# Optimization experiments

Measured on AMD Instinct MI355X. Metric: run time of the kernel, lower is better.

Reference implementation:

```python
import jax, jax.numpy as jnp
import numpy as np

BETA_VQ = 0.25
NUM_CODES = 1024
CODE_DIM = 256

def setup_inputs() -> dict:
    key = jax.random.key(0)
    k1, k2 = jax.random.split(key)
    z_e = jax.random.normal(k1, (64, 32, 32, CODE_DIM), dtype=jnp.float32)
    codebook = jax.random.uniform(k2, (NUM_CODES, CODE_DIM), dtype=jnp.float32,
                                  minval=-1.0 / NUM_CODES, maxval=1.0 / NUM_CODES)
    return {"z_e": z_e, "codebook": codebook}


def reference(z_e, codebook):
    B, H, W, D = z_e.shape
    z_flat = z_e.reshape(-1, D)  # [N, D], N = B*H*W
    # squared-euclidean distances via expansion: ||z||^2 + ||c||^2 - 2 z.c
    dist = (jnp.sum(z_flat ** 2, axis=1, keepdims=True)
            + jnp.sum(codebook ** 2, axis=1)
            - 2.0 * z_flat @ codebook.T)  # [N, num_codes]
    indices = jnp.argmin(dist, axis=1)  # [N]
    z_q = codebook[indices].reshape(z_e.shape)  # [B,H,W,D]
    codebook_loss = jnp.mean((jax.lax.stop_gradient(z_e) - z_q) ** 2)
    commit_loss = BETA_VQ * jnp.mean((z_e - jax.lax.stop_gradient(z_q)) ** 2)
    vq_loss = codebook_loss + commit_loss
    z_q_st = z_e + jax.lax.stop_gradient(z_q - z_e)  # straight-through
    indices = indices.reshape(B, H, W)
    return (z_q_st, vq_loss, indices)
```

## Files before the change

kernel.cpp:

```cpp
#include <hip/hip_runtime.h>
#include <hip/hip_bf16.h>


constexpr int D     = 256;
constexpr int NC    = 1024;
constexpr int NROWS = 65536;
constexpr int RPB   = 32;
constexpr int NBLK  = NROWS / RPB;
constexpr int ZS    = 264;
constexpr int QCAP  = 1024;
#define MARGIN_Q 3.8e-3f

typedef float accv4  __attribute__((ext_vector_type(4)));
typedef short short8 __attribute__((ext_vector_type(8)));

__device__ __forceinline__ short f2bf(float x) {
    __hip_bfloat16 h = __float2bfloat16(x);
    return *reinterpret_cast<short*>(&h);
}
__device__ __forceinline__ unsigned packtrunc(float x, float y) {
    return (__float_as_uint(x) >> 16) | (__float_as_uint(y) & 0xffff0000u);
}

__device__ __forceinline__ float np_pairwise_sq128(const float* __restrict__ x) {
    float r[8];
    #pragma unroll
    for (int j = 0; j < 8; ++j) r[j] = __fmul_rn(x[j], x[j]);
    #pragma unroll
    for (int i = 8; i < 128; i += 8)
        #pragma unroll
        for (int j = 0; j < 8; ++j)
            r[j] = __fadd_rn(r[j], __fmul_rn(x[i + j], x[i + j]));
    float s01 = __fadd_rn(r[0], r[1]);
    float s23 = __fadd_rn(r[2], r[3]);
    float s45 = __fadd_rn(r[4], r[5]);
    float s67 = __fadd_rn(r[6], r[7]);
    return __fadd_rn(__fadd_rn(s01, s23), __fadd_rn(s45, s67));
}

__global__ void c2_kernel(const float* __restrict__ cb, float* __restrict__ c2) {
    int t = blockIdx.x * blockDim.x + threadIdx.x;
    if (t < NC) {
        const float* x = cb + (size_t)t * D;
        c2[t] = __fadd_rn(np_pairwise_sq128(x), np_pairwise_sq128(x + 128));
    }
}

__global__ void swz_kernel(const float* __restrict__ cb, short* __restrict__ swz) {
    int t = blockIdx.x * blockDim.x + threadIdx.x;
    int lane = t & 63, ts = t >> 6;
    int ks = ts & 7, tile = ts >> 3;
    int code = tile * 16 + (lane & 15);
    int kb   = ks * 32 + (lane >> 4) * 8;
    const float* src = cb + (size_t)code * D + kb;
    union { short s[8]; short8 v; } u;
    #pragma unroll
    for (int j = 0; j < 8; ++j) u.s[j] = f2bf(src[j]);
    *((short8*)swz + t) = u.v;
}

__global__ __launch_bounds__(256, 2) void vq_kernel(
    const float* __restrict__ z,
    const float* __restrict__ cb,
    const short* __restrict__ cb_swz,
    const float* __restrict__ c2g,
    float*       __restrict__ out_zq,
    float*       __restrict__ out_idx,
    double*      __restrict__ partials)
{
    __shared__ __align__(16) float z_lds[RPB][ZS];
    __shared__ float a_row[RPB];
    __shared__ __align__(16) float scratchA[RPB][4];
    __shared__ float c2_lds[NC];
    __shared__ int   rm_shared[RPB];
    __shared__ __align__(16) int queue[QCAP];
    __shared__ int   qn;

    const int tid     = threadIdx.x;
    const int lane    = tid & 63;
    const int w       = tid >> 6;
    const int rowBase = blockIdx.x * RPB;

    #pragma unroll
    for (int j = 0; j < 8; ++j) {
        int l = tid + 256 * j;
        int row = l >> 6, q = l & 63;
        float4 v = *(const float4*)(z + (size_t)(rowBase + row) * D + q * 4);
        *(float4*)&z_lds[row][q * 4] = v;
    }
    #pragma unroll
    for (int j = 0; j < 4; ++j) c2_lds[tid + 256 * j] = c2g[tid + 256 * j];
    if (tid < RPB) rm_shared[tid] = 0x7f800000;
    if (tid == 0)  qn = 0;
    __syncthreads();

    if (tid < RPB * 4) {
        int row = tid >> 2, q = tid & 3;
        int h = (q >> 1) * 128, p = (q & 1) * 4;
        const float* x = &z_lds[row][0];
        float r0 = __fmul_rn(x[h+p+0], x[h+p+0]);
        float r1 = __fmul_rn(x[h+p+1], x[h+p+1]);
        float r2 = __fmul_rn(x[h+p+2], x[h+p+2]);
        float r3 = __fmul_rn(x[h+p+3], x[h+p+3]);
        #pragma unroll
        for (int i = 8; i < 128; i += 8) {
            r0 = __fadd_rn(r0, __fmul_rn(x[h+i+p+0], x[h+i+p+0]));
            r1 = __fadd_rn(r1, __fmul_rn(x[h+i+p+1], x[h+i+p+1]));
            r2 = __fadd_rn(r2, __fmul_rn(x[h+i+p+2], x[h+i+p+2]));
            r3 = __fadd_rn(r3, __fmul_rn(x[h+i+p+3], x[h+i+p+3]));
        }
        scratchA[row][q] = __fadd_rn(__fadd_rn(r0, r1), __fadd_rn(r2, r3));
    }
    __syncthreads();
    if (tid < RPB) {
        float half0 = __fadd_rn(scratchA[tid][0], scratchA[tid][1]);
        float half1 = __fadd_rn(scratchA[tid][2], scratchA[tid][3]);
        a_row[tid]  = __fadd_rn(half0, half1);
    }
    __syncthreads();

    short8 afrag[2][8];
    #pragma unroll
    for (int rt = 0; rt < 2; ++rt)
        #pragma unroll
        for (int ks = 0; ks < 8; ++ks) {
            const float* src = z + (size_t)(rowBase + rt * 16 + (lane & 15)) * D
                                 + ks * 32 + (lane >> 4) * 8;
            float4 v0 = *(const float4*)(src);
            float4 v1 = *(const float4*)(src + 4);
            union { unsigned u[4]; short8 v; } pk;
            pk.u[0] = packtrunc(v0.x, v0.y);
            pk.u[1] = packtrunc(v0.z, v0.w);
            pk.u[2] = packtrunc(v1.x, v1.y);
            pk.u[3] = packtrunc(v1.z, v1.w);
            afrag[rt][ks] = pk.v;
        }
    float a_reg[2][4];
    #pragma unroll
    for (int rt = 0; rt < 2; ++rt)
        #pragma unroll
        for (int i = 0; i < 4; ++i)
            a_reg[rt][i] = a_row[rt * 16 + (lane >> 4) * 4 + i];

    float runmin[2][4];
    #pragma unroll
    for (int rt = 0; rt < 2; ++rt)
        #pragma unroll
        for (int i = 0; i < 4; ++i) runmin[rt][i] = 3.4e38f;

    const short8* bbase = (const short8*)cb_swz + lane;
    short8 bcur[8];
    #pragma unroll
    for (int ks = 0; ks < 8; ++ks) bcur[ks] = bbase[(size_t)w * 512 + ks * 64];

    unsigned kpk[2][2][2];
    #pragma unroll
    for (int t = 0; t < 2; ++t) {
        const int tile = w + 4 * t;
        short8 bnxt[8];
        #pragma unroll
        for (int ks = 0; ks < 8; ++ks)
            bnxt[ks] = bbase[(size_t)(tile + 4) * 512 + ks * 64];
        accv4 acc[2];
        #pragma unroll
        for (int rt = 0; rt < 2; ++rt) acc[rt] = (accv4){0.f, 0.f, 0.f, 0.f};
        #pragma unroll
        for (int ks = 0; ks < 8; ++ks) {
            #pragma unroll
            for (int rt = 0; rt < 2; ++rt)
                acc[rt] = __builtin_amdgcn_mfma_f32_16x16x32_bf16(
                    afrag[rt][ks], bcur[ks], acc[rt], 0, 0, 0);
        }
        const float c2v = c2_lds[tile * 16 + (lane & 15)];
        #pragma unroll
        for (int rt = 0; rt < 2; ++rt) {
            float m0 = fmaf(2.0f, acc[rt][0], -c2v);
            float m1 = fmaf(2.0f, acc[rt][1], -c2v);
            float m2 = fmaf(2.0f, acc[rt][2], -c2v);
            float m3 = fmaf(2.0f, acc[rt][3], -c2v);
            kpk[t][rt][0] = packtrunc(m0, m1);
            kpk[t][rt][1] = packtrunc(m2, m3);
            runmin[rt][0] = fminf(runmin[rt][0], a_reg[rt][0] - m0);
            runmin[rt][1] = fminf(runmin[rt][1], a_reg[rt][1] - m1);
            runmin[rt][2] = fminf(runmin[rt][2], a_reg[rt][2] - m2);
            runmin[rt][3] = fminf(runmin[rt][3], a_reg[rt][3] - m3);
        }
        #pragma unroll
        for (int ks = 0; ks < 8; ++ks) bcur[ks] = bnxt[ks];
    }

    #pragma unroll
    for (int rt = 0; rt < 2; ++rt)
        #pragma unroll
        for (int i = 0; i < 4; ++i) {
            float m = runmin[rt][i];
            m = fminf(m, __shfl_xor(m, 1));
            m = fminf(m, __shfl_xor(m, 2));
            m = fminf(m, __shfl_xor(m, 4));
            m = fminf(m, __shfl_xor(m, 8));
            if ((lane & 15) == 0) {
                int row = rt * 16 + (lane >> 4) * 4 + i;
                atomicMin(&rm_shared[row], __float_as_int(m));
            }
        }
    __syncthreads();

    float mthr[2][4];
    #pragma unroll
    for (int rt = 0; rt < 2; ++rt)
        #pragma unroll
        for (int i = 0; i < 4; ++i) {
            int row = rt * 16 + (lane >> 4) * 4 + i;
            mthr[rt][i] = a_reg[rt][i]
                        - (__int_as_float(rm_shared[row]) + MARGIN_Q);
        }

    #pragma unroll
    for (int t = 0; t < 2; ++t) {
        const int code = (w + 4 * t) * 16 + (lane & 15);
        #pragma unroll
        for (int rt = 0; rt < 2; ++rt)
            #pragma unroll
            for (int pr = 0; pr < 2; ++pr) {
                unsigned pk = kpk[t][rt][pr];
                float mlo = __uint_as_float(pk << 16);
                float mhi = __uint_as_float(pk & 0xffff0000u);
                if (mlo >= mthr[rt][2 * pr]) {
                    int row  = rt * 16 + (lane >> 4) * 4 + 2 * pr;
                    int slot = atomicAdd(&qn, 1);
                    if (slot < QCAP) queue[slot] = (row << 10) | code;
                }
                if (mhi >= mthr[rt][2 * pr + 1]) {
                    int row  = rt * 16 + (lane >> 4) * 4 + 2 * pr + 1;
                    int slot = atomicAdd(&qn, 1);
                    if (slot < QCAP) queue[slot] = (row << 10) | code;
                }
            }
    }

    for (int t = 2; t < 16; ++t) {
        const int tile = w + 4 * t;
        short8 bnxt[8];
        if (t < 15) {
            #pragma unroll
            for (int ks = 0; ks < 8; ++ks)
                bnxt[ks] = bbase[(size_t)(tile + 4) * 512 + ks * 64];
        }
        accv4 acc[2];
        #pragma unroll
        for (int rt = 0; rt < 2; ++rt) acc[rt] = (accv4){0.f, 0.f, 0.f, 0.f};
        #pragma unroll
        for (int ks = 0; ks < 8; ++ks) {
            #pragma unroll
            for (int rt = 0; rt < 2; ++rt)
                acc[rt] = __builtin_amdgcn_mfma_f32_16x16x32_bf16(
                    afrag[rt][ks], bcur[ks], acc[rt], 0, 0, 0);
        }
        const float c2v  = c2_lds[tile * 16 + (lane & 15)];
        const int   code = tile * 16 + (lane & 15);
        #pragma unroll
        for (int rt = 0; rt < 2; ++rt) {
            #pragma unroll
            for (int i = 0; i < 4; ++i) {
                float m = fmaf(2.0f, acc[rt][i], -c2v);
                runmin[rt][i] = fminf(runmin[rt][i], a_reg[rt][i] - m);
                if (m >= mthr[rt][i]) {
                    int row  = rt * 16 + (lane >> 4) * 4 + i;
                    int slot = atomicAdd(&qn, 1);
                    if (slot < QCAP) queue[slot] = (row << 10) | code;
                }
            }
        }
        if (t == 5 || t == 9 || t == 13) {
            #pragma unroll
            for (int rt = 0; rt < 2; ++rt)
                #pragma unroll
                for (int i = 0; i < 4; ++i) {
                    float m = runmin[rt][i];
                    m = fminf(m, __shfl_xor(m, 1));
                    m = fminf(m, __shfl_xor(m, 2));
                    m = fminf(m, __shfl_xor(m, 4));
                    m = fminf(m, __shfl_xor(m, 8));
                    if ((lane & 15) == 0) {
                        int row = rt * 16 + (lane >> 4) * 4 + i;
                        atomicMin(&rm_shared[row], __float_as_int(m));
                    }
                }
            #pragma unroll
            for (int rt = 0; rt < 2; ++rt)
                #pragma unroll
                for (int i = 0; i < 4; ++i) {
                    int row = rt * 16 + (lane >> 4) * 4 + i;
                    mthr[rt][i] = a_reg[rt][i]
                                - (__int_as_float(rm_shared[row]) + MARGIN_Q);
                }
        }
        if (t < 15) {
            #pragma unroll
            for (int ks = 0; ks < 8; ++ks) bcur[ks] = bnxt[ks];
        }
    }

    unsigned long long* best64 = (unsigned long long*)&scratchA[0][0];
    if (tid < RPB) best64[tid] = ~0ull;
    __syncthreads();
    int total = qn;
    if (total <= QCAP) {
        for (int t = tid; t < total; t += 256) {
            int e = queue[t];
            int row = e >> 10, code = e & 1023;
            const float4* cp = (const float4*)(cb + (size_t)code * D);
            const float*  zr = &z_lds[row][0];
            float acc = 0.0f;
            #pragma unroll 8
            for (int d4 = 0; d4 < 64; ++d4) {
                float4 cv = cp[d4];
                acc = fmaf(zr[d4 * 4 + 0], cv.x, acc);
                acc = fmaf(zr[d4 * 4 + 1], cv.y, acc);
                acc = fmaf(zr[d4 * 4 + 2], cv.z, acc);
                acc = fmaf(zr[d4 * 4 + 3], cv.w, acc);
            }
            float key = __fsub_rn(__fadd_rn(a_row[row], c2_lds[code]), 2.0f * acc);
            unsigned long long pk =
                ((unsigned long long)__float_as_uint(key) << 32) | (unsigned)code;
            atomicMin(&best64[row], pk);
        }
    } else {
        for (int r = 0; r < RPB; ++r) {
            for (int c = tid; c < NC; c += 256) {
                const float4* cp = (const float4*)(cb + (size_t)c * D);
                const float*  zr = &z_lds[r][0];
                float acc = 0.0f;
                #pragma unroll 8
                for (int d4 = 0; d4 < 64; ++d4) {
                    float4 cv = cp[d4];
                    acc = fmaf(zr[d4 * 4 + 0], cv.x, acc);
                    acc = fmaf(zr[d4 * 4 + 1], cv.y, acc);
                    acc = fmaf(zr[d4 * 4 + 2], cv.z, acc);
                    acc = fmaf(zr[d4 * 4 + 3], cv.w, acc);
                }
                float key = __fsub_rn(__fadd_rn(a_row[r], c2_lds[c]), 2.0f * acc);
                unsigned long long pk =
                    ((unsigned long long)__float_as_uint(key) << 32) | (unsigned)c;
                atomicMin(&best64[r], pk);
            }
        }
    }
    __syncthreads();

    int* winner = rm_shared;
    if (tid < RPB) {
        unsigned long long b = best64[tid];
        int wdx = (b == ~0ull) ? 0 : (int)(b & 0xffffffffu);
        winner[tid] = wdx;
        out_idx[rowBase + tid] = (float)wdx;
    }
    __syncthreads();

    double lacc = 0.0;
    #pragma unroll
    for (int j = 0; j < 8; ++j) {
        int idx = tid + 256 * j;
        int row = idx >> 6;
        int q4  = idx & 63;
        int wd  = winner[row];
        float4 cv = *(const float4*)(cb + (size_t)wd * D + q4 * 4);
        float4 zv = *(const float4*)&z_lds[row][q4 * 4];
        float4 o;
        o.x = __fadd_rn(zv.x, __fsub_rn(cv.x, zv.x));
        o.y = __fadd_rn(zv.y, __fsub_rn(cv.y, zv.y));
        o.z = __fadd_rn(zv.z, __fsub_rn(cv.z, zv.z));
        o.w = __fadd_rn(zv.w, __fsub_rn(cv.w, zv.w));
        *(float4*)(out_zq + (size_t)(rowBase + row) * D + q4 * 4) = o;
        double d0 = (double)zv.x - (double)cv.x;
        double d1 = (double)zv.y - (double)cv.y;
        double d2 = (double)zv.z - (double)cv.z;
        double d3 = (double)zv.w - (double)cv.w;
        lacc += d0 * d0 + d1 * d1 + d2 * d2 + d3 * d3;
    }
    __syncthreads();
    double* dred = (double*)&queue[0];
    dred[tid] = lacc;
    __syncthreads();
    for (int s = 128; s > 0; s >>= 1) {
        if (tid < s) dred[tid] += dred[tid + s];
        __syncthreads();
    }
    if (tid == 0) partials[blockIdx.x] = dred[0];
}

__global__ void loss_kernel(const double* __restrict__ partials,
                            float* __restrict__ out_loss)
{
    __shared__ double sm[256];
    int tid = threadIdx.x;
    double s = 0.0;
    for (int i = tid; i < NBLK; i += 256) s += partials[i];
    sm[tid] = s;
    __syncthreads();
    for (int k = 128; k > 0; k >>= 1) {
        if (tid < k) sm[tid] += sm[tid + k];
        __syncthreads();
    }
    if (tid == 0)
        out_loss[0] = (float)(1.25 * sm[0] / (double)((size_t)NROWS * D));
}

extern "C" void kernel_launch(void* const* d_in, const int* in_sizes, int n_in,
                              void* d_out, int out_size, void* d_ws, size_t ws_size,
                              hipStream_t stream)
{
    const float* z  = (const float*)d_in[0];
    const float* cb = (const float*)d_in[1];

    float* out      = (float*)d_out;
    float* out_zq   = out;
    float* out_loss = out + (size_t)NROWS * D;
    float* out_idx  = out_loss + 1;

    char*   ws       = (char*)d_ws;
    short*  cb_swz   = (short*)ws;
    float*  c2       = (float*)(ws + 524288);
    double* partials = (double*)(ws + 528384);

    swz_kernel<<<128, 256, 0, stream>>>(cb, cb_swz);
    c2_kernel<<<4, 256, 0, stream>>>(cb, c2);
    vq_kernel<<<NBLK, 256, 0, stream>>>(z, cb, cb_swz, c2,
                                        out_zq, out_idx, partials);
    loss_kernel<<<1, 256, 0, stream>>>(partials, out_loss);
}
```

Measured before the change: 279.4 us.

## Drop z LDS staging, read z from global, raise occupancy to four blocks

Removes the 33 KB shared-memory copy of the z tile and reads z rows directly from global memory (relying on cache) for the norm, rescoring and output phases. With LDS use cut, launch bounds go from 2 to 4 blocks per CU to raise occupancy. The periodic mid-loop running-min threshold refresh is also removed, so the candidate threshold is no longer tightened during the scan. This can enqueue more candidates and overflow the queue into the slow full-rescore fallback, and register pressure at 4 blocks may cause spills.

```diff
diff --git a/kernel.cpp b/kernel.cpp
--- a/kernel.cpp
+++ b/kernel.cpp
@@ -7,7 +7,6 @@
 constexpr int NROWS = 65536;
 constexpr int RPB   = 32;
 constexpr int NBLK  = NROWS / RPB;
-constexpr int ZS    = 264;
 constexpr int QCAP  = 1024;
 #define MARGIN_Q 3.8e-3f
 
@@ -59,7 +58,7 @@
     *((short8*)swz + t) = u.v;
 }
 
-__global__ __launch_bounds__(256, 2) void vq_kernel(
+__global__ __launch_bounds__(256, 4) void vq_kernel(
     const float* __restrict__ z,
     const float* __restrict__ cb,
     const short* __restrict__ cb_swz,
@@ -68,10 +67,9 @@
     float*       __restrict__ out_idx,
     double*      __restrict__ partials)
 {
-    __shared__ __align__(16) float z_lds[RPB][ZS];
+    __shared__ float c2_lds[NC];
     __shared__ float a_row[RPB];
     __shared__ __align__(16) float scratchA[RPB][4];
-    __shared__ float c2_lds[NC];
     __shared__ int   rm_shared[RPB];
     __shared__ __align__(16) int queue[QCAP];
     __shared__ int   qn;
@@ -82,42 +80,9 @@
     const int rowBase = blockIdx.x * RPB;
 
     #pragma unroll
-    for (int j = 0; j < 8; ++j) {
-        int l = tid + 256 * j;
-        int row = l >> 6, q = l & 63;
-        float4 v = *(const float4*)(z + (size_t)(rowBase + row) * D + q * 4);
-        *(float4*)&z_lds[row][q * 4] = v;
-    }
-    #pragma unroll
     for (int j = 0; j < 4; ++j) c2_lds[tid + 256 * j] = c2g[tid + 256 * j];
     if (tid < RPB) rm_shared[tid] = 0x7f800000;
     if (tid == 0)  qn = 0;
-    __syncthreads();
-
-    if (tid < RPB * 4) {
-        int row = tid >> 2, q = tid & 3;
-        int h = (q >> 1) * 128, p = (q & 1) * 4;
-        const float* x = &z_lds[row][0];
-        float r0 = __fmul_rn(x[h+p+0], x[h+p+0]);
-        float r1 = __fmul_rn(x[h+p+1], x[h+p+1]);
-        float r2 = __fmul_rn(x[h+p+2], x[h+p+2]);
-        float r3 = __fmul_rn(x[h+p+3], x[h+p+3]);
-        #pragma unroll
-        for (int i = 8; i < 128; i += 8) {
-            r0 = __fadd_rn(r0, __fmul_rn(x[h+i+p+0], x[h+i+p+0]));
-            r1 = __fadd_rn(r1, __fmul_rn(x[h+i+p+1], x[h+i+p+1]));
-            r2 = __fadd_rn(r2, __fmul_rn(x[h+i+p+2], x[h+i+p+2]));
-            r3 = __fadd_rn(r3, __fmul_rn(x[h+i+p+3], x[h+i+p+3]));
-        }
-        scratchA[row][q] = __fadd_rn(__fadd_rn(r0, r1), __fadd_rn(r2, r3));
-    }
-    __syncthreads();
-    if (tid < RPB) {
-        float half0 = __fadd_rn(scratchA[tid][0], scratchA[tid][1]);
-        float half1 = __fadd_rn(scratchA[tid][2], scratchA[tid][3]);
-        a_row[tid]  = __fadd_rn(half0, half1);
-    }
-    __syncthreads();
 
     short8 afrag[2][8];
     #pragma unroll
@@ -135,6 +100,32 @@
             pk.u[3] = packtrunc(v1.z, v1.w);
             afrag[rt][ks] = pk.v;
         }
+
+    if (tid < RPB * 4) {
+        int row = tid >> 2, q = tid & 3;
+        int h = (q >> 1) * 128, p = (q & 1) * 4;
+        const float* x = z + (size_t)(rowBase + row) * D;
+        float r0 = __fmul_rn(x[h+p+0], x[h+p+0]);
+        float r1 = __fmul_rn(x[h+p+1], x[h+p+1]);
+        float r2 = __fmul_rn(x[h+p+2], x[h+p+2]);
+        float r3 = __fmul_rn(x[h+p+3], x[h+p+3]);
+        #pragma unroll
+        for (int i = 8; i < 128; i += 8) {
+            r0 = __fadd_rn(r0, __fmul_rn(x[h+i+p+0], x[h+i+p+0]));
+            r1 = __fadd_rn(r1, __fmul_rn(x[h+i+p+1], x[h+i+p+1]));
+            r2 = __fadd_rn(r2, __fmul_rn(x[h+i+p+2], x[h+i+p+2]));
+            r3 = __fadd_rn(r3, __fmul_rn(x[h+i+p+3], x[h+i+p+3]));
+        }
+        scratchA[row][q] = __fadd_rn(__fadd_rn(r0, r1), __fadd_rn(r2, r3));
+    }
+    __syncthreads();
+    if (tid < RPB) {
+        float half0 = __fadd_rn(scratchA[tid][0], scratchA[tid][1]);
+        float half1 = __fadd_rn(scratchA[tid][2], scratchA[tid][3]);
+        a_row[tid]  = __fadd_rn(half0, half1);
+    }
+    __syncthreads();
+
     float a_reg[2][4];
     #pragma unroll
     for (int rt = 0; rt < 2; ++rt)
@@ -271,30 +262,6 @@
                 }
             }
         }
-        if (t == 5 || t == 9 || t == 13) {
-            #pragma unroll
-            for (int rt = 0; rt < 2; ++rt)
-                #pragma unroll
-                for (int i = 0; i < 4; ++i) {
-                    float m = runmin[rt][i];
-                    m = fminf(m, __shfl_xor(m, 1));
-                    m = fminf(m, __shfl_xor(m, 2));
-                    m = fminf(m, __shfl_xor(m, 4));
-                    m = fminf(m, __shfl_xor(m, 8));
-                    if ((lane & 15) == 0) {
-                        int row = rt * 16 + (lane >> 4) * 4 + i;
-                        atomicMin(&rm_shared[row], __float_as_int(m));
-                    }
-                }
-            #pragma unroll
-            for (int rt = 0; rt < 2; ++rt)
-                #pragma unroll
-                for (int i = 0; i < 4; ++i) {
-                    int row = rt * 16 + (lane >> 4) * 4 + i;
-                    mthr[rt][i] = a_reg[rt][i]
-                                - (__int_as_float(rm_shared[row]) + MARGIN_Q);
-                }
-        }
         if (t < 15) {
             #pragma unroll
             for (int ks = 0; ks < 8; ++ks) bcur[ks] = bnxt[ks];
@@ -310,7 +277,7 @@
             int e = queue[t];
             int row = e >> 10, code = e & 1023;
             const float4* cp = (const float4*)(cb + (size_t)code * D);
-            const float*  zr = &z_lds[row][0];
+            const float*  zr = z + (size_t)(rowBase + row) * D;
             float acc = 0.0f;
             #pragma unroll 8
             for (int d4 = 0; d4 < 64; ++d4) {
@@ -329,7 +296,7 @@
         for (int r = 0; r < RPB; ++r) {
             for (int c = tid; c < NC; c += 256) {
                 const float4* cp = (const float4*)(cb + (size_t)c * D);
-                const float*  zr = &z_lds[r][0];
+                const float*  zr = z + (size_t)(rowBase + r) * D;
                 float acc = 0.0f;
                 #pragma unroll 8
                 for (int d4 = 0; d4 < 64; ++d4) {
@@ -365,7 +332,7 @@
         int q4  = idx & 63;
         int wd  = winner[row];
         float4 cv = *(const float4*)(cb + (size_t)wd * D + q4 * 4);
-        float4 zv = *(const float4*)&z_lds[row][q4 * 4];
+        float4 zv = *(const float4*)(z + (size_t)(rowBase + row) * D + q4 * 4);
         float4 o;
         o.x = __fadd_rn(zv.x, __fsub_rn(cv.x, zv.x));
         o.y = __fadd_rn(zv.y, __fsub_rn(cv.y, zv.y));
```

Result: slower. 444.1 us (+59.0%).
